# Kernel optimization log

Hardware: AMD Instinct MI355X
Metric: run time of the kernel (lower is better)

## Reference

```python
import jax, jax.numpy as jnp
import numpy as np

# ---- constants (match init_kwargs / input_specs) ----
B, NPG, EPG = 512, 50, 60          # graphs, nodes/graph, edges/graph
D, V = 128, 100000                 # embedding_dim, num_items
SPLITS, SCALE = 4, 12.0            # euler steps, logit scale
N, E = B * NPG, B * EPG
STDV = 1.0 / np.sqrt(D)


def _seg_sum(vals, idx, n):
    return jax.ops.segment_sum(vals, idx, num_segments=n)


def _l2norm(x, eps=1e-12):
    return x / jnp.maximum(jnp.linalg.norm(x, axis=-1, keepdims=True), eps)


def setup_inputs() -> dict:
    key = jax.random.key(0)
    ks = jax.random.split(key, 40)
    u = lambda i, shape: jax.random.uniform(ks[i], shape, minval=-STDV, maxval=STDV, dtype=jnp.float32)
    offs = jnp.repeat(jnp.arange(B, dtype=jnp.int32) * NPG, EPG)
    inp = dict(
        iid=jax.random.randint(ks[0], (N,), 0, V),
        src=jax.random.randint(ks[1], (E,), 0, NPG).astype(jnp.int32) + offs,
        dst=jax.random.randint(ks[2], (E,), 0, NPG).astype(jnp.int32) + offs,
        edge_w=jax.random.uniform(ks[3], (E,), minval=0.1, maxval=1.0, dtype=jnp.float32),
        edge_t=jax.random.uniform(ks[4], (E,), dtype=jnp.float32),
        node_t=jax.random.uniform(ks[5], (N,), dtype=jnp.float32),
        emb=u(6, (V, D)),
        # GGNN layer (num_layers=1): W1, W2 and torch-layout GRUCell(2D -> D)
        W1=u(7, (D, D)), W2=u(8, (D, D)),
        gw_ih=u(9, (3 * D, 2 * D)), gw_hh=u(10, (3 * D, D)),
        gb_ih=u(11, (3 * D,)), gb_hh=u(12, (3 * D,)),
        # GraphGRUODE GCNConv weights (x@W + b), norm='both'
        Wxr=u(13, (D, D)), bxr=u(14, (D,)), Wxz=u(15, (D, D)), bxz=u(16, (D,)),
        Wxh=u(17, (D, D)), bxh=u(18, (D,)), Whr=u(19, (D, D)), bhr=u(20, (D,)),
        Whz=u(21, (D, D)), bhz=u(22, (D,)), Whh=u(23, (D, D)), bhh=u(24, (D,)),
        # AttnReadout
        Wu=u(25, (D, D)), Wv=u(26, (D, D)), bv=u(27, (D,)), We=u(28, (D, 1)),
        # fc_sr: [2D -> D], no bias
        W_sr=u(29, (2 * D, D)),
    )
    return inp


def reference(iid, src, dst, edge_w, edge_t, node_t, emb,
              W1, W2, gw_ih, gw_hh, gb_ih, gb_hh,
              Wxr, bxr, Wxz, bxz, Wxh, bxh, Whr, bhr, Whz, bhz, Whh, bhh,
              Wu, Wv, bv, We, W_sr):
    # ---- embedding + normalize ----
    feat = _l2norm(emb[iid])                                   # [N, D]

    # ---- GGNNLayer: weighted mean over in-edges, both directions, GRU cell ----
    wcol = edge_w[:, None]
    num1 = _seg_sum(feat[src] * wcol, dst, N)
    den1 = _seg_sum(edge_w, dst, N)
    neigh1 = num1 / jnp.where(den1 == 0, 1.0, den1)[:, None]    # zero for isolated nodes
    num2 = _seg_sum(feat[dst] * wcol, src, N)
    den2 = _seg_sum(edge_w, src, N)
    neigh2 = num2 / jnp.where(den2 == 0, 1.0, den2)[:, None]
    hn = jnp.concatenate([neigh1 @ W1, neigh2 @ W2], axis=1)    # [N, 2D]
    gi = hn @ gw_ih.T + gb_ih
    gh = feat @ gw_hh.T + gb_hh
    ir, iz, ig = jnp.split(gi, 3, axis=1)
    hr, hz, hg = jnp.split(gh, 3, axis=1)
    r = jax.nn.sigmoid(ir + hr)
    z = jax.nn.sigmoid(iz + hz)
    g = jnp.tanh(ig + r * hg)
    feat = (1.0 - z) * g + z * feat
    feat = _l2norm(feat)

    # ---- GraphGRUODE: euler integration over dynamic masked subgraphs ----
    x = feat
    t_end = edge_t.max()
    dt = t_end / SPLITS
    nodiag = src != dst

    def ode_f(t, h):
        nm = node_t >= t                                        # node subgraph mask
        em = (edge_t <= t) & nm[src] & nm[dst] & nodiag          # edge mask (no self-loops)
        emf = em.astype(h.dtype)
        deg = _seg_sum(emf, src, N) + _seg_sum(emf, dst, N)      # undirected degree (reverse edges added)
        dis = jnp.clip(deg, 1.0, None) ** -0.5

        def conv(inp, W, b):                                     # GCNConv, norm='both'
            s = inp * dis[:, None]
            agg = (_seg_sum(s[src] * emf[:, None], dst, N)
                   + _seg_sum(s[dst] * emf[:, None], src, N))
            return (agg * dis[:, None]) @ W + b

        rr = jax.nn.sigmoid(conv(x, Wxr, bxr) + conv(h, Whr, bhr))
        zz = jax.nn.sigmoid(conv(x, Wxz, bxz) + conv(h, Whz, bhz))
        uu = jnp.tanh(conv(x, Wxh, bxh) + conv(rr * h, Whh, bhh))
        dh = (1.0 - zz) * (uu - h)
        return jnp.where(nm[:, None], dh, 0.0)

    h = x
    for k in range(SPLITS):
        h = h + dt * ode_f(k * dt, h)
    feat = _l2norm(h)

    # ---- AttnReadout (fixed NPG nodes/graph -> reshape as segment ops) ----
    fb = feat.reshape(B, NPG, D)
    last = fb[:, -1, :]                                          # last node of each session
    e = jax.nn.sigmoid(fb @ Wu + (last @ Wv + bv)[:, None, :]) @ We   # [B, NPG, 1]
    alpha = jax.nn.softmax(e, axis=1)
    sr_g = jnp.sum(fb * alpha, axis=1)                           # [B, D]

    sr = _l2norm(jnp.concatenate([last, sr_g], axis=1) @ W_sr)   # [B, D]
    target = _l2norm(emb)                                        # [V, D]
    logits = sr @ target.T                                       # [B, V]
    return jax.nn.log_softmax(SCALE * logits, axis=-1)
```

## Files before the change

### kernel.cpp

```cpp
#include <hip/hip_runtime.h>

#define BB 512
#define NPG 50
#define EPG 60
#define DD 128
#define VV 100000
#define VPAD 100032
#define NSPLITS 4
#define FSCALE 12.0f
#define NN (BB*NPG)
#define EE (BB*EPG)
#define NDTOT (NN*DD)
#define NCB (VPAD/64)

typedef __attribute__((ext_vector_type(8))) short bfx8;
typedef __attribute__((ext_vector_type(4))) float f32x4;

__device__ __forceinline__ float sigmoidf_(float x){ return 1.f/(1.f+expf(-x)); }
__device__ __forceinline__ short f2bf(float f){
  union { float f; unsigned u; } v; v.f = f;
  unsigned r = v.u + 0x7FFF + ((v.u >> 16) & 1);
  return (short)(r >> 16);
}

__global__ __launch_bounds__(256) void k_embn(const float* __restrict__ emb, short* __restrict__ embn) {
  int row = blockIdx.x*4 + (threadIdx.x >> 6);
  int lane = threadIdx.x & 63;
  if (row >= VPAD) return;
  if (row >= VV) { embn[(size_t)row*DD+lane]=0; embn[(size_t)row*DD+64+lane]=0; return; }
  const float* r = emb + (size_t)row*DD;
  float a = r[lane], b = r[lane+64];
  float s = a*a + b*b;
  for (int off=32; off; off>>=1) s += __shfl_down(s, off);
  s = __shfl(s, 0);
  float inv = 1.0f/fmaxf(sqrtf(s), 1e-12f);
  embn[(size_t)row*DD+lane]    = f2bf(a*inv);
  embn[(size_t)row*DD+64+lane] = f2bf(b*inv);
}

__global__ __launch_bounds__(128) void k_gather(const int* __restrict__ iid, const float* __restrict__ emb,
                                                float* __restrict__ x, short* __restrict__ xb) {
  int n = blockIdx.x, d = threadIdx.x;
  int v = iid[n];
  float e = emb[(size_t)v*DD + d];
  __shared__ float red2[2];
  float ss = e*e;
  for (int off=32; off; off>>=1) ss += __shfl_down(ss, off);
  if ((d & 63)==0) red2[d>>6] = ss;
  __syncthreads();
  float inv = 1.f/fmaxf(sqrtf(red2[0]+red2[1]), 1e-12f);
  float f = e*inv;
  x[(size_t)n*DD + d] = f;
  xb[(size_t)n*DD + d] = f2bf(f);
}

__global__ __launch_bounds__(256) void k_dt(const float* __restrict__ edge_t, float* __restrict__ dtp) {
  __shared__ float red[256];
  float m = -1e30f;
  for (int e = threadIdx.x; e < EE; e += 256) m = fmaxf(m, edge_t[e]);
  red[threadIdx.x] = m; __syncthreads();
  for (int s=128; s; s>>=1){ if ((int)threadIdx.x < s) red[threadIdx.x] = fmaxf(red[threadIdx.x], red[threadIdx.x+s]); __syncthreads(); }
  if (threadIdx.x==0) dtp[0] = red[0] / (float)NSPLITS;
}

__global__ void k_m12t(const float* __restrict__ W1, const float* __restrict__ W2,
                       const float* __restrict__ gw_ih, short* __restrict__ M12t) {
  int c = blockIdx.x, k = threadIdx.x;
  const float* Wrow = (k < 128) ? (W1 + (size_t)k*128) : (W2 + (size_t)(k-128)*128);
  const float* grow = gw_ih + (size_t)c*256 + ((k < 128) ? 0 : 128);
  float s = 0.f;
  for (int j = 0; j < 128; ++j) s += Wrow[j]*grow[j];
  M12t[(size_t)c*256 + k] = f2bf(s);
}
__global__ void k_bfcopy(const float* __restrict__ src, short* __restrict__ dst) {
  size_t i = (size_t)blockIdx.x*blockDim.x + threadIdx.x;
  dst[i] = f2bf(src[i]);
}
__global__ void k_wrzt(const float* __restrict__ Wxr, const float* __restrict__ Wxz,
                       const float* __restrict__ Whr, const float* __restrict__ Whz,
                       short* __restrict__ Wrzt) {
  int c = blockIdx.x, k = threadIdx.x;
  float v;
  if (k < 128) v = (c < 128) ? Wxr[k*128+c] : Wxz[k*128+(c-128)];
  else         v = (c < 128) ? Whr[(k-128)*128+c] : Whz[(k-128)*128+(c-128)];
  Wrzt[(size_t)c*256 + k] = f2bf(v);
}
__global__ void k_wu2t(const float* __restrict__ Wxh, const float* __restrict__ Whh, short* __restrict__ Wu2t) {
  int c = blockIdx.x, k = threadIdx.x;
  float v = (k < 128) ? Wxh[k*128+c] : Whh[(k-128)*128+c];
  Wu2t[(size_t)c*256 + k] = f2bf(v);
}
__global__ void k_wt128(const float* __restrict__ W, short* __restrict__ Wt) {
  int c = blockIdx.x, k = threadIdx.x;
  Wt[(size_t)c*128 + k] = f2bf(W[(size_t)k*128 + c]);
}
__global__ void k_build_bias(const float* __restrict__ bxr, const float* __restrict__ bhr,
                             const float* __restrict__ bxz, const float* __restrict__ bhz,
                             const float* __restrict__ bxh, const float* __restrict__ bhh,
                             float* __restrict__ brz, float* __restrict__ bu) {
  int t = threadIdx.x;
  if (t < 128) brz[t] = bxr[t] + bhr[t];
  else if (t < 256) brz[t] = bxz[t-128] + bhz[t-128];
  else bu[t-256] = bxh[t-256] + bhh[t-256];
}

__global__ __launch_bounds__(256) void k_grp_mean(const int* __restrict__ src, const int* __restrict__ dst,
                                                  const float* __restrict__ ew, const float* __restrict__ feat,
                                                  short* __restrict__ ABb) {
  __shared__ float fl[NPG*128];
  __shared__ float n1[NPG*128];
  __shared__ float n2[NPG*128];
  __shared__ int sl[EPG], tl[EPG];
  __shared__ float wl[EPG];
  __shared__ float d1[NPG], d2[NPG];
  int b = blockIdx.x, tid = threadIdx.x;
  int nb = b*NPG, eb = b*EPG;
  for (int i = tid; i < NPG*32; i += 256) {
    ((float4*)fl)[i] = ((const float4*)(feat + (size_t)nb*128))[i];
    ((float4*)n1)[i] = make_float4(0.f,0.f,0.f,0.f);
    ((float4*)n2)[i] = make_float4(0.f,0.f,0.f,0.f);
  }
  if (tid < EPG) { sl[tid] = src[eb+tid]-nb; tl[tid] = dst[eb+tid]-nb; wl[tid] = ew[eb+tid]; }
  __syncthreads();
  const int dgrp = tid >> 7, d = tid & 127;
  if (dgrp == 0) {
    for (int e = 0; e < EPG; ++e) n1[tl[e]*128+d] += fl[sl[e]*128+d]*wl[e];
  } else {
    for (int e = 0; e < EPG; ++e) n2[sl[e]*128+d] += fl[tl[e]*128+d]*wl[e];
  }
  if (tid < NPG) {
    float den = 0.f;
    for (int e = 0; e < EPG; ++e) den += (tl[e]==tid) ? wl[e] : 0.f;
    d1[tid] = (den == 0.f) ? 1.f : den;
  } else if (tid >= 128 && tid < 128+NPG) {
    int dd = tid - 128;
    float den = 0.f;
    for (int e = 0; e < EPG; ++e) den += (sl[e]==dd) ? wl[e] : 0.f;
    d2[dd] = (den == 0.f) ? 1.f : den;
  }
  __syncthreads();
  for (int n = 0; n < NPG; ++n) {
    float v = dgrp ? (n2[n*128+d]/d2[n]) : (n1[n*128+d]/d1[n]);
    ABb[(size_t)(nb+n)*256 + dgrp*128 + d] = f2bf(v);
  }
}

__global__ __launch_bounds__(128) void k_gru(const float* __restrict__ gi, const float* __restrict__ gh,
                                             float* __restrict__ x) {
  int n = blockIdx.x, d = threadIdx.x;
  const float* gin = gi + (size_t)n*384;
  const float* ghn = gh + (size_t)n*384;
  float ir = gin[d], iz = gin[128+d], ig = gin[256+d];
  float hr = ghn[d], hz = ghn[128+d], hg = ghn[256+d];
  float f0 = x[(size_t)n*DD + d];
  float r = sigmoidf_(ir + hr);
  float z = sigmoidf_(iz + hz);
  float g = tanhf(ig + r*hg);
  float f = (1.f - z)*g + z*f0;
  __shared__ float red2[2];
  float ss = f*f;
  for (int off=32; off; off>>=1) ss += __shfl_down(ss, off);
  if ((d & 63)==0) red2[d>>6] = ss;
  __syncthreads();
  float inv = 1.f/fmaxf(sqrtf(red2[0]+red2[1]), 1e-12f);
  x[(size_t)n*DD + d] = f*inv;
}

__global__ __launch_bounds__(256) void k_ode_fused(
    const int* __restrict__ src, const int* __restrict__ dst,
    const float* __restrict__ edge_t, const float* __restrict__ node_t,
    const float* __restrict__ dtp,
    float* __restrict__ x, short* __restrict__ fbb,
    const short* __restrict__ Wrzt, const short* __restrict__ Wu2t,
    const float* __restrict__ brz, const float* __restrict__ bu)
{
  __shared__ __align__(16) float xl[NPG*128];
  __shared__ __align__(16) float hl[NPG*128];
  __shared__ __align__(16) float S1[NPG*128];
  __shared__ __align__(16) float S2[NPG*128];
  __shared__ __align__(16) float zzl[NPG*128];
  __shared__ __align__(16) short aggX[64*136];
  __shared__ __align__(16) short aggH[64*136];
  __shared__ int stl[EPG];
  __shared__ float etl[EPG];
  __shared__ float ntl[NPG];
  __shared__ float disl[NPG];
  __shared__ unsigned long long actm_s;
  __shared__ float red4[4];

  const int b = blockIdx.x, tid = threadIdx.x;
  const int nb = b*NPG, eb = b*EPG;
  const int wave = tid>>6, lane = tid&63, quad = lane>>4, l16 = lane&15;
  const float dtv = dtp[0];

  for (int i = tid; i < NPG*32; i += 256) {
    float4 v = ((const float4*)(x + (size_t)nb*128))[i];
    ((float4*)xl)[i] = v;
    ((float4*)hl)[i] = v;
  }
  if (tid < EPG) { stl[tid] = (src[eb+tid]-nb) | ((dst[eb+tid]-nb)<<16); etl[tid] = edge_t[eb+tid]; }
  if (tid >= 64 && tid < 64+NPG) ntl[tid-64] = node_t[nb+tid-64];
  for (int i = tid; i < 14*136; i += 256) { aggX[50*136 + i] = 0; aggH[50*136 + i] = 0; }
  __syncthreads();

  for (int ks = 0; ks < NSPLITS; ++ks) {
    const float t = (float)ks * dtv;
    if (wave == 0) {
      bool p = false;
      if (lane < EPG) {
        int st = stl[lane]; int s = st & 0xffff, tt = st >> 16;
        p = (etl[lane] <= t) && (ntl[s] >= t) && (ntl[tt] >= t) && (s != tt);
      }
      unsigned long long m = __ballot(p);
      if (lane == 0) actm_s = m;
    }
    for (int i = tid; i < NPG*128; i += 256) { S1[i] = 0.f; S2[i] = 0.f; }
    __syncthreads();
    const unsigned long long actm = actm_s;
    if (tid < NPG) {
      float deg = 0.f;
      for (int e = 0; e < EPG; ++e) {
        if ((actm >> e) & 1ULL) {
          int st = stl[e]; int s = st & 0xffff, tt = st >> 16;
          deg += (s==tid ? 1.f:0.f) + (tt==tid ? 1.f:0.f);
        }
      }
      disl[tid] = rsqrtf(fmaxf(deg, 1.f));
    }
    __syncthreads();
    if (tid < 128) {
      const int d = tid;
      for (int e = 0; e < EPG; ++e) {
        if ((actm >> e) & 1ULL) {
          int st = stl[e]; int s = st & 0xffff, tt = st >> 16;
          float ds_ = disl[s], dt_ = disl[tt];
          S1[tt*128+d] += xl[s*128+d]*ds_;
          S1[s*128+d]  += xl[tt*128+d]*dt_;
          S2[tt*128+d] += hl[s*128+d]*ds_;
          S2[s*128+d]  += hl[tt*128+d]*dt_;
        }
      }
    }
    __syncthreads();
    for (int i = tid; i < NPG*128; i += 256) {
      int r = i >> 7, c = i & 127;
      aggX[r*136 + c] = f2bf(S1[i]*disl[r]);
      aggH[r*136 + c] = f2bf(S2[i]*disl[r]);
    }
    __syncthreads();
    {
      f32x4 acc[4][4] = {{{0.f,0.f,0.f,0.f},{0.f,0.f,0.f,0.f},{0.f,0.f,0.f,0.f},{0.f,0.f,0.f,0.f}},
                         {{0.f,0.f,0.f,0.f},{0.f,0.f,0.f,0.f},{0.f,0.f,0.f,0.f},{0.f,0.f,0.f,0.f}},
                         {{0.f,0.f,0.f,0.f},{0.f,0.f,0.f,0.f},{0.f,0.f,0.f,0.f},{0.f,0.f,0.f,0.f}},
                         {{0.f,0.f,0.f,0.f},{0.f,0.f,0.f,0.f},{0.f,0.f,0.f,0.f},{0.f,0.f,0.f,0.f}}};
      for (int k0 = 0; k0 < 256; k0 += 32) {
        const short* Ab = (k0 < 128) ? aggX : aggH;
        const int kk = (k0 & 127) + quad*8;
        bfx8 af[4];
#pragma unroll
        for (int m = 0; m < 4; ++m) af[m] = *(const bfx8*)&Ab[(m*16+l16)*136 + kk];
#pragma unroll
        for (int n = 0; n < 4; ++n) {
          const int bn = (wave*4+n)*16 + l16;
          bfx8 bf = *(const bfx8*)&Wrzt[(size_t)bn*256 + k0 + quad*8];
#pragma unroll
          for (int m = 0; m < 4; ++m)
            acc[m][n] = __builtin_amdgcn_mfma_f32_16x16x32_bf16(af[m], bf, acc[m][n], 0, 0, 0);
        }
      }
#pragma unroll
      for (int n = 0; n < 4; ++n) {
        const int col = (wave*4+n)*16 + l16;
        const float bb = brz[col];
#pragma unroll
        for (int m = 0; m < 4; ++m)
#pragma unroll
          for (int r = 0; r < 4; ++r) {
            const int row = m*16 + quad*4 + r;
            if (row < NPG) {
              float s = sigmoidf_(acc[m][n][r] + bb);
              if (col < 128) S1[row*128+col] = s * hl[row*128+col];
              else           zzl[row*128+col-128] = s;
            }
          }
      }
    }
    __syncthreads();
    for (int i = tid; i < NPG*128; i += 256) S2[i] = 0.f;
    __syncthreads();
    if (tid < 128) {
      const int d = tid;
      for (int e = 0; e < EPG; ++e) {
        if ((actm >> e) & 1ULL) {
          int st = stl[e]; int s = st & 0xffff, tt = st >> 16;
          S2[tt*128+d] += S1[s*128+d]*disl[s];
          S2[s*128+d]  += S1[tt*128+d]*disl[tt];
        }
      }
    }
    __syncthreads();
    for (int i = tid; i < NPG*128; i += 256) {
      int r = i >> 7, c = i & 127;
      aggH[r*136 + c] = f2bf(S2[i]*disl[r]);
    }
    __syncthreads();
    {
      f32x4 acc[4][2] = {{{0.f,0.f,0.f,0.f},{0.f,0.f,0.f,0.f}},
                         {{0.f,0.f,0.f,0.f},{0.f,0.f,0.f,0.f}},
                         {{0.f,0.f,0.f,0.f},{0.f,0.f,0.f,0.f}},
                         {{0.f,0.f,0.f,0.f},{0.f,0.f,0.f,0.f}}};
      for (int k0 = 0; k0 < 256; k0 += 32) {
        const short* Ab = (k0 < 128) ? aggX : aggH;
        const int kk = (k0 & 127) + quad*8;
        bfx8 af[4];
#pragma unroll
        for (int m = 0; m < 4; ++m) af[m] = *(const bfx8*)&Ab[(m*16+l16)*136 + kk];
#pragma unroll
        for (int n = 0; n < 2; ++n) {
          const int bn = (wave*2+n)*16 + l16;
          bfx8 bf = *(const bfx8*)&Wu2t[(size_t)bn*256 + k0 + quad*8];
#pragma unroll
          for (int m = 0; m < 4; ++m)
            acc[m][n] = __builtin_amdgcn_mfma_f32_16x16x32_bf16(af[m], bf, acc[m][n], 0, 0, 0);
        }
      }
#pragma unroll
      for (int n = 0; n < 2; ++n) {
        const int col = (wave*2+n)*16 + l16;
        const float bb = bu[col];
#pragma unroll
        for (int m = 0; m < 4; ++m)
#pragma unroll
          for (int r = 0; r < 4; ++r) {
            const int row = m*16 + quad*4 + r;
            if (row < NPG && ntl[row] >= t) {
              float hv = hl[row*128+col];
              float uu = tanhf(acc[m][n][r] + bb);
              float zv = zzl[row*128+col];
              hl[row*128+col] = hv + dtv*(1.f - zv)*(uu - hv);
            }
          }
      }
    }
    __syncthreads();
  }

  for (int rp = 0; rp < NPG; rp += 2) {
    const int r = rp + (tid>>7);
    const int d = tid & 127;
    float v = hl[r*128 + d];
    float ss = v*v;
    for (int off=32; off; off>>=1) ss += __shfl_down(ss, off);
    if (lane == 0) red4[wave] = ss;
    __syncthreads();
    int w0 = (tid>>7)*2;
    float inv = 1.f/fmaxf(sqrtf(red4[w0]+red4[w0+1]), 1e-12f);
    float f = v*inv;
    x[(size_t)(nb+r)*128 + d] = f;
    fbb[(size_t)(nb+r)*128 + d] = f2bf(f);
    __syncthreads();
  }
}

__global__ __launch_bounds__(256) void gemm_mfma(
    const short* __restrict__ A, int lda,
    const short* __restrict__ Bt, int ldbt,
    const float* __restrict__ bias,
    float* __restrict__ C, int ldc,
    int K, int mode,
    float* __restrict__ outp, float* __restrict__ pmax, float* __restrict__ psum)
{
  __shared__ short As[64*40];
  __shared__ short Bs[64*40];
  const int tid = threadIdx.x;
  const int wave = tid >> 6, lane = tid & 63;
  const int wr = wave >> 1, wc = wave & 1;
  const int quad = lane >> 4, l16 = lane & 15;
  int rb, cb;
  if (mode >= 4) {
    int t = (blockIdx.x & 7)*1563 + (blockIdx.x >> 3);
    rb = t & 7; cb = t >> 3;
  } else { rb = blockIdx.y; cb = blockIdx.x; }
  const int row0 = rb*64, col0 = cb*64;
  f32x4 acc[2][2] = {{{0.f,0.f,0.f,0.f},{0.f,0.f,0.f,0.f}},{{0.f,0.f,0.f,0.f},{0.f,0.f,0.f,0.f}}};
  const int sm = tid >> 2, skq = tid & 3;
  const short* Ap = A + (size_t)(row0+sm)*lda + skq*8;
  const short* Bp = Bt + (size_t)(col0+sm)*ldbt + skq*8;
  for (int k0 = 0; k0 < K; k0 += 32) {
    *(bfx8*)&As[sm*40 + skq*8] = *(const bfx8*)(Ap + k0);
    *(bfx8*)&Bs[sm*40 + skq*8] = *(const bfx8*)(Bp + k0);
    __syncthreads();
    bfx8 a0 = *(bfx8*)&As[(wr*32 + l16)*40 + quad*8];
    bfx8 a1 = *(bfx8*)&As[(wr*32 + 16 + l16)*40 + quad*8];
    bfx8 b0 = *(bfx8*)&Bs[(wc*32 + l16)*40 + quad*8];
    bfx8 b1 = *(bfx8*)&Bs[(wc*32 + 16 + l16)*40 + quad*8];
    acc[0][0] = __builtin_amdgcn_mfma_f32_16x16x32_bf16(a0, b0, acc[0][0], 0, 0, 0);
    acc[0][1] = __builtin_amdgcn_mfma_f32_16x16x32_bf16(a0, b1, acc[0][1], 0, 0, 0);
    acc[1][0] = __builtin_amdgcn_mfma_f32_16x16x32_bf16(a1, b0, acc[1][0], 0, 0, 0);
    acc[1][1] = __builtin_amdgcn_mfma_f32_16x16x32_bf16(a1, b1, acc[1][1], 0, 0, 0);
    __syncthreads();
  }

  if (mode == 0) {
#pragma unroll
    for (int i = 0; i < 2; ++i)
#pragma unroll
      for (int j = 0; j < 2; ++j) {
        int gc = col0 + wc*32 + j*16 + l16;
        float bb = bias ? bias[gc] : 0.f;
#pragma unroll
        for (int r = 0; r < 4; ++r) {
          int gr = row0 + wr*32 + i*16 + quad*4 + r;
          C[(size_t)gr*ldc + gc] = acc[i][j][r] + bb;
        }
      }
  } else if (mode == 4) {
    __shared__ float pm[64][2], ps[64][2];
    int c0 = col0 + wc*32 + l16;
    int c1 = c0 + 16;
#pragma unroll
    for (int i = 0; i < 2; ++i) {
#pragma unroll
      for (int r = 0; r < 4; ++r) {
        int rloc = wr*32 + i*16 + quad*4 + r;
        float v0 = (c0 < VV) ? acc[i][0][r] : -1e30f;
        float v1 = (c1 < VV) ? acc[i][1][r] : -1e30f;
        float m = fmaxf(v0, v1);
#pragma unroll
        for (int off = 1; off < 16; off <<= 1) m = fmaxf(m, __shfl_xor(m, off));
        float s = expf(v0 - m) + expf(v1 - m);
#pragma unroll
        for (int off = 1; off < 16; off <<= 1) s += __shfl_xor(s, off);
        if (l16 == 0) { pm[rloc][wc] = m; ps[rloc][wc] = s; }
      }
    }
    __syncthreads();
    if (tid < 64) {
      float m0 = pm[tid][0], m1 = pm[tid][1];
      float s0 = ps[tid][0], s1 = ps[tid][1];
      float M = fmaxf(m0, m1);
      float S = s0*expf(m0 - M) + s1*expf(m1 - M);
      pmax[(size_t)(row0 + tid)*NCB + cb] = M;
      psum[(size_t)(row0 + tid)*NCB + cb] = S;
    }
  } else {
#pragma unroll
    for (int i = 0; i < 2; ++i) {
#pragma unroll
      for (int r = 0; r < 4; ++r) {
        int gr = row0 + wr*32 + i*16 + quad*4 + r;
        float l = bias[gr];
#pragma unroll
        for (int j = 0; j < 2; ++j) {
          int gc = col0 + wc*32 + j*16 + l16;
          if (gc < VV) outp[(size_t)gr*VV + gc] = acc[i][j][r] - l;
        }
      }
    }
  }
}

__global__ __launch_bounds__(128) void k_attn(const float* __restrict__ fb, const float* __restrict__ U,
                                              const float* __restrict__ lv, const float* __restrict__ We,
                                              const float* __restrict__ W_sr, short* __restrict__ srvb) {
  int b = blockIdx.x, d = threadIdx.x;
  __shared__ float sc[NPG];
  __shared__ float lastv[DD], srg[DD];
  __shared__ float red2[2];
  const float* Ub  = U  + (size_t)b*NPG*DD;
  const float* lvb = lv + (size_t)b*DD;
  if (d < 64) {
    for (int i=0;i<NPG;++i) {
      float e = We[d]   * sigmoidf_(Ub[i*DD + d]      + lvb[d]) +
                We[d+64]* sigmoidf_(Ub[i*DD + 64 + d] + lvb[d+64]);
      for (int off=32; off; off>>=1) e += __shfl_down(e, off);
      if (d==0) sc[i] = e;
    }
  }
  __syncthreads();
  if (d < 64) {
    float v = (d < NPG) ? sc[d] : -1e30f;
    float m = v;
    for (int off=1; off<64; off<<=1) m = fmaxf(m, __shfl_xor(m, off));
    float ex = (d < NPG) ? expf(v - m) : 0.f;
    float s = ex;
    for (int off=1; off<64; off<<=1) s += __shfl_xor(s, off);
    if (d < NPG) sc[d] = ex/s;
  }
  __syncthreads();
  const float* fbb = fb + (size_t)b*NPG*DD;
  float lastd = fbb[(NPG-1)*DD + d];
  float sg = 0.f;
  for (int i=0;i<NPG;++i) sg += fbb[i*DD + d]*sc[i];
  lastv[d] = lastd; srg[d] = sg;
  __syncthreads();
  float acc = 0.f;
  for (int k=0;k<DD;++k) acc += lastv[k]*W_sr[k*DD + d];
  for (int k=0;k<DD;++k) acc += srg[k]*W_sr[(DD+k)*DD + d];
  float ss = acc*acc;
  for (int off=32; off; off>>=1) ss += __shfl_down(ss, off);
  if ((d & 63)==0) red2[d>>6] = ss;
  __syncthreads();
  float inv = 1.f/fmaxf(sqrtf(red2[0]+red2[1]), 1e-12f);
  srvb[(size_t)b*DD + d] = f2bf(FSCALE*acc*inv);
}

__global__ __launch_bounds__(256) void k_lse(const float* __restrict__ pmax, const float* __restrict__ psum,
                                             float* __restrict__ lse) {
  int r = blockIdx.x, tid = threadIdx.x;
  float m = -1e30f, s = 0.f;
  for (int cb = tid; cb < NCB; cb += 256) {
    float m2 = pmax[(size_t)r*NCB + cb], s2 = psum[(size_t)r*NCB + cb];
    float M = fmaxf(m, m2);
    s = s*expf(m - M) + s2*expf(m2 - M);
    m = M;
  }
  __shared__ float ms[256], ssh[256];
  ms[tid] = m; ssh[tid] = s; __syncthreads();
  for (int st=128; st; st>>=1) {
    if (tid < st) {
      float m2 = ms[tid+st], s2 = ssh[tid+st];
      float M = fmaxf(ms[tid], m2);
      ssh[tid] = ssh[tid]*expf(ms[tid]-M) + s2*expf(m2-M);
      ms[tid] = M;
    }
    __syncthreads();
  }
  if (tid==0) lse[r] = ms[0] + logf(ssh[0]);
}

extern "C" void kernel_launch(void* const* d_in, const int* in_sizes, int n_in,
                              void* d_out, int out_size, void* d_ws, size_t ws_size,
                              hipStream_t stream) {
  (void)in_sizes; (void)n_in; (void)out_size; (void)ws_size;
  const int*   iid    = (const int*)  d_in[0];
  const int*   src    = (const int*)  d_in[1];
  const int*   dst    = (const int*)  d_in[2];
  const float* edge_w = (const float*)d_in[3];
  const float* edge_t = (const float*)d_in[4];
  const float* node_t = (const float*)d_in[5];
  const float* emb    = (const float*)d_in[6];
  const float* W1     = (const float*)d_in[7];
  const float* W2     = (const float*)d_in[8];
  const float* gw_ih  = (const float*)d_in[9];
  const float* gw_hh  = (const float*)d_in[10];
  const float* gb_ih  = (const float*)d_in[11];
  const float* gb_hh  = (const float*)d_in[12];
  const float* Wxr = (const float*)d_in[13]; const float* bxr = (const float*)d_in[14];
  const float* Wxz = (const float*)d_in[15]; const float* bxz = (const float*)d_in[16];
  const float* Wxh = (const float*)d_in[17]; const float* bxh = (const float*)d_in[18];
  const float* Whr = (const float*)d_in[19]; const float* bhr = (const float*)d_in[20];
  const float* Whz = (const float*)d_in[21]; const float* bhz = (const float*)d_in[22];
  const float* Whh = (const float*)d_in[23]; const float* bhh = (const float*)d_in[24];
  const float* Wu  = (const float*)d_in[25];
  const float* Wv  = (const float*)d_in[26]; const float* bv  = (const float*)d_in[27];
  const float* We  = (const float*)d_in[28];
  const float* W_sr= (const float*)d_in[29];

  float* ws  = (float*)d_ws;
  float* out = (float*)d_out;

  short* embn = (short*)ws;
  float* pmax = ws + 6402048;
  float* psum = pmax + 800256;
  short* M12t = (short*)(psum + 800256);
  short* gwhhb= (short*)(psum + 800256 + 49152);
  short* Wrzt = (short*)(psum + 800256 + 73728);
  short* Wu2t = (short*)(psum + 800256 + 106496);
  short* Wut  = (short*)(psum + 800256 + 122880);
  short* Wvt  = (short*)(psum + 800256 + 131072);
  float* brz  = psum + 800256 + 139264;
  float* bu   = brz + 256;
  float* lv   = bu + 128;
  float* dtp  = lv + 65536;
  float* lse  = dtp + 4;
  short* srvb = (short*)(lse + 512);

  short* ABb = (short*)out;
  float* x   = out + (size_t) 4*1024*1024;
  float* gi  = out + (size_t)20*1024*1024;
  float* gh  = out + (size_t)30*1024*1024;
  float* U   = out + (size_t)20*1024*1024;
  short* xb  = (short*)(out + (size_t)40*1024*1024);
  short* fbb = (short*)(out + (size_t)42*1024*1024);

  k_embn<<<VPAD/4, 256, 0, stream>>>(emb, embn);
  k_gather<<<NN, 128, 0, stream>>>(iid, emb, x, xb);
  k_dt<<<1, 256, 0, stream>>>(edge_t, dtp);
  k_m12t<<<384, 256, 0, stream>>>(W1, W2, gw_ih, M12t);
  k_bfcopy<<<384, 128, 0, stream>>>(gw_hh, gwhhb);
  k_wrzt<<<256, 256, 0, stream>>>(Wxr, Wxz, Whr, Whz, Wrzt);
  k_wu2t<<<128, 256, 0, stream>>>(Wxh, Whh, Wu2t);
  k_wt128<<<128, 128, 0, stream>>>(Wu, Wut);
  k_wt128<<<128, 128, 0, stream>>>(Wv, Wvt);
  k_build_bias<<<1, 384, 0, stream>>>(bxr, bhr, bxz, bhz, bxh, bhh, brz, bu);

  k_grp_mean<<<BB, 256, 0, stream>>>(src, dst, edge_w, x, ABb);

  gemm_mfma<<<dim3(6,400), 256, 0, stream>>>(ABb, 256, M12t, 256, gb_ih, gi, 384, 256, 0,
      nullptr, nullptr, nullptr);
  gemm_mfma<<<dim3(6,400), 256, 0, stream>>>(xb, 128, gwhhb, 128, gb_hh, gh, 384, 128, 0,
      nullptr, nullptr, nullptr);
  k_gru<<<NN, 128, 0, stream>>>(gi, gh, x);

  k_ode_fused<<<BB, 256, 0, stream>>>(src, dst, edge_t, node_t, dtp, x, fbb, Wrzt, Wu2t, brz, bu);

  gemm_mfma<<<dim3(2,400), 256, 0, stream>>>(fbb, 128, Wut, 128, nullptr, U, 128, 128, 0,
      nullptr, nullptr, nullptr);
  gemm_mfma<<<dim3(2,8), 256, 0, stream>>>(fbb + (size_t)(NPG-1)*DD, NPG*DD, Wvt, 128, bv, lv, 128, 128, 0,
      nullptr, nullptr, nullptr);
  k_attn<<<BB, 128, 0, stream>>>(x, U, lv, We, W_sr, srvb);

  gemm_mfma<<<dim3(8*NCB), 256, 0, stream>>>(srvb, 128, embn, 128, nullptr, nullptr, 0, 128, 4,
      nullptr, pmax, psum);
  k_lse<<<BB, 256, 0, stream>>>(pmax, psum, lse);
  gemm_mfma<<<dim3(8*NCB), 256, 0, stream>>>(srvb, 128, embn, 128, lse, nullptr, 0, 128, 5,
      out, nullptr, nullptr);
}
```

Baseline: 813.5 us.

## Reorder GCN ODE as transform-then-aggregate with precomputed x-projections

The ODE kernel now multiplies the weights first (h@W) and then aggregates with a small dense normalized adjacency matrix built in LDS via MFMA, instead of doing per-edge scatter sums over 128-wide features followed by a 256-K GEMM. The x-side projections (x@Wxr, Wxz, Wxh) are constant across Euler steps, so they are hoisted into one bf16 GEMM before the kernel. The block grows to 512 threads and LDS use drops, which should remove the serial edge loops run by only 128 threads. The cost is extra bf16 rounding (adjacency matrix accumulated in bf16, intermediates stored as bf16) and one more global GEMM launch.

```diff
diff --git a/kernel.cpp b/kernel.cpp
--- a/kernel.cpp
+++ b/kernel.cpp
@@ -10,8 +10,11 @@
 #define FSCALE 12.0f
 #define NN (BB*NPG)
 #define EE (BB*EPG)
-#define NDTOT (NN*DD)
 #define NCB (VPAD/64)
+#define HSTR 132
+#define RSTR 136
+#define TSTR 72
+#define MSTR 72
 
 typedef __attribute__((ext_vector_type(8))) short bfx8;
 typedef __attribute__((ext_vector_type(4))) float f32x4;
@@ -21,6 +24,19 @@
   union { float f; unsigned u; } v; v.f = f;
   unsigned r = v.u + 0x7FFF + ((v.u >> 16) & 1);
   return (short)(r >> 16);
+}
+__device__ __forceinline__ float bf2f(short s){
+  union { unsigned u; float f; } v; v.u = ((unsigned)(unsigned short)s) << 16;
+  return v.f;
+}
+__device__ __forceinline__ unsigned cvtpk_(float lo, float hi){
+  unsigned r; asm("v_cvt_pk_bf16_f32 %0, %1, %2" : "=v"(r) : "v"(lo), "v"(hi)); return r;
+}
+__device__ __forceinline__ bfx8 pack8(float4 a, float4 b){
+  union { bfx8 v; unsigned u[4]; } w;
+  w.u[0] = cvtpk_(a.x, a.y); w.u[1] = cvtpk_(a.z, a.w);
+  w.u[2] = cvtpk_(b.x, b.y); w.u[3] = cvtpk_(b.z, b.w);
+  return w.v;
 }
 
 __global__ __launch_bounds__(256) void k_embn(const float* __restrict__ emb, short* __restrict__ embn) {
@@ -76,19 +92,19 @@
   size_t i = (size_t)blockIdx.x*blockDim.x + threadIdx.x;
   dst[i] = f2bf(src[i]);
 }
-__global__ void k_wrzt(const float* __restrict__ Wxr, const float* __restrict__ Wxz,
-                       const float* __restrict__ Whr, const float* __restrict__ Whz,
-                       short* __restrict__ Wrzt) {
+__global__ void k_whrzt(const float* __restrict__ Whr, const float* __restrict__ Whz,
+                        short* __restrict__ Whrzt) {
   int c = blockIdx.x, k = threadIdx.x;
-  float v;
-  if (k < 128) v = (c < 128) ? Wxr[k*128+c] : Wxz[k*128+(c-128)];
-  else         v = (c < 128) ? Whr[(k-128)*128+c] : Whz[(k-128)*128+(c-128)];
-  Wrzt[(size_t)c*256 + k] = f2bf(v);
-}
-__global__ void k_wu2t(const float* __restrict__ Wxh, const float* __restrict__ Whh, short* __restrict__ Wu2t) {
+  float v = (c < 128) ? Whr[(size_t)k*128 + c] : Whz[(size_t)k*128 + (c-128)];
+  Whrzt[(size_t)c*128 + k] = f2bf(v);
+}
+__global__ void k_w3t(const float* __restrict__ Wxr, const float* __restrict__ Wxz,
+                      const float* __restrict__ Wxh, short* __restrict__ W3t) {
   int c = blockIdx.x, k = threadIdx.x;
-  float v = (k < 128) ? Wxh[k*128+c] : Whh[(k-128)*128+c];
-  Wu2t[(size_t)c*256 + k] = f2bf(v);
+  float v = (c < 128) ? Wxr[(size_t)k*128 + c]
+          : (c < 256) ? Wxz[(size_t)k*128 + (c-128)]
+                      : Wxh[(size_t)k*128 + (c-256)];
+  W3t[(size_t)c*128 + k] = f2bf(v);
 }
 __global__ void k_wt128(const float* __restrict__ W, short* __restrict__ Wt) {
   int c = blockIdx.x, k = threadIdx.x;
@@ -146,7 +162,7 @@
 }
 
 __global__ __launch_bounds__(128) void k_gru(const float* __restrict__ gi, const float* __restrict__ gh,
-                                             float* __restrict__ x) {
+                                             float* __restrict__ x, short* __restrict__ xb2) {
   int n = blockIdx.x, d = threadIdx.x;
   const float* gin = gi + (size_t)n*384;
   const float* ghn = gh + (size_t)n*384;
@@ -163,45 +179,150 @@
   if ((d & 63)==0) red2[d>>6] = ss;
   __syncthreads();
   float inv = 1.f/fmaxf(sqrtf(red2[0]+red2[1]), 1e-12f);
-  x[(size_t)n*DD + d] = f*inv;
-}
-
-__global__ __launch_bounds__(256) void k_ode_fused(
+  float out = f*inv;
+  x[(size_t)n*DD + d] = out;
+  xb2[(size_t)n*DD + d] = f2bf(out);
+}
+
+__global__ __launch_bounds__(512, 4) void k_ode_fused(
     const int* __restrict__ src, const int* __restrict__ dst,
     const float* __restrict__ edge_t, const float* __restrict__ node_t,
     const float* __restrict__ dtp,
     float* __restrict__ x, short* __restrict__ fbb,
-    const short* __restrict__ Wrzt, const short* __restrict__ Wu2t,
+    const short* __restrict__ XA,
+    const short* __restrict__ Whrzt, const short* __restrict__ Whht,
     const float* __restrict__ brz, const float* __restrict__ bu)
 {
-  __shared__ __align__(16) float xl[NPG*128];
-  __shared__ __align__(16) float hl[NPG*128];
-  __shared__ __align__(16) float S1[NPG*128];
-  __shared__ __align__(16) float S2[NPG*128];
-  __shared__ __align__(16) float zzl[NPG*128];
-  __shared__ __align__(16) short aggX[64*136];
-  __shared__ __align__(16) short aggH[64*136];
-  __shared__ int stl[EPG];
+  __shared__ __align__(16) float hl[NPG*HSTR];
+  __shared__ __align__(16) short rhb[NPG*RSTR];
+  __shared__ __align__(16) short T1t[128*TSTR];
+  __shared__ __align__(16) short Mp[64*MSTR];
+  __shared__ int   rp[NPG+1];
+  __shared__ short ci[2*EPG];
+  __shared__ int   cnt[NPG];
+  __shared__ int   stl[EPG];
   __shared__ float etl[EPG];
   __shared__ float ntl[NPG];
   __shared__ float disl[NPG];
   __shared__ unsigned long long actm_s;
-  __shared__ float red4[4];
+  __shared__ float red8[8];
 
   const int b = blockIdx.x, tid = threadIdx.x;
   const int nb = b*NPG, eb = b*EPG;
   const int wave = tid>>6, lane = tid&63, quad = lane>>4, l16 = lane&15;
   const float dtv = dtp[0];
 
-  for (int i = tid; i < NPG*32; i += 256) {
-    float4 v = ((const float4*)(x + (size_t)nb*128))[i];
-    ((float4*)xl)[i] = v;
-    ((float4*)hl)[i] = v;
+  for (int i = tid; i < NPG*32; i += 512) {
+    int n = i >> 5, dq = i & 31;
+    ((float4*)(hl + n*HSTR))[dq] = ((const float4*)(x + (size_t)(nb+n)*128))[dq];
   }
   if (tid < EPG) { stl[tid] = (src[eb+tid]-nb) | ((dst[eb+tid]-nb)<<16); etl[tid] = edge_t[eb+tid]; }
   if (tid >= 64 && tid < 64+NPG) ntl[tid-64] = node_t[nb+tid-64];
-  for (int i = tid; i < 14*136; i += 256) { aggX[50*136 + i] = 0; aggH[50*136 + i] = 0; }
-  __syncthreads();
+  __syncthreads();
+
+  if (tid < NPG) {
+    int c = 0;
+    for (int e = 0; e < EPG; ++e) { int st=stl[e]; int s=st&0xffff, t=st>>16; c += (s==tid)+(t==tid); }
+    cnt[tid] = c;
+  }
+  __syncthreads();
+  if (tid == 0) { int a = 0; for (int n = 0; n < NPG; ++n) { rp[n] = a; a += cnt[n]; } rp[NPG] = a; }
+  __syncthreads();
+  if (tid < NPG) {
+    int w = rp[tid];
+    for (int e = 0; e < EPG; ++e) {
+      int st = stl[e]; int s = st & 0xffff, t = st >> 16;
+      if (t == tid) ci[w++] = (short)(s | (e<<8));
+      if (s == tid) ci[w++] = (short)(t | (e<<8));
+    }
+  }
+  __syncthreads();
+
+  float zreg[4][4];
+
+#define HW_PHASE(WT, XAOFS, USERH)                                                   \
+  {                                                                                  \
+    f32x4 acc[4] = {{0.f,0.f,0.f,0.f},{0.f,0.f,0.f,0.f},{0.f,0.f,0.f,0.f},{0.f,0.f,0.f,0.f}}; \
+    const int coln = wave*16 + l16;                                                  \
+    _Pragma("unroll")                                                                \
+    for (int k0 = 0; k0 < 128; k0 += 32) {                                           \
+      bfx8 af[4];                                                                    \
+      _Pragma("unroll")                                                              \
+      for (int m = 0; m < 4; ++m) {                                                  \
+        int arow = m*16 + l16; if (arow > NPG-1) arow = NPG-1;                       \
+        if (USERH) {                                                                 \
+          af[m] = *(const bfx8*)&rhb[arow*RSTR + k0 + quad*8];                       \
+        } else {                                                                     \
+          const float* hp = &hl[arow*HSTR + k0 + quad*8];                            \
+          float4 f0 = *(const float4*)hp;                                            \
+          float4 f1 = *(const float4*)(hp+4);                                        \
+          af[m] = pack8(f0, f1);                                                     \
+        }                                                                            \
+      }                                                                              \
+      bfx8 bfr = *(const bfx8*)&(WT)[(size_t)coln*128 + k0 + quad*8];                \
+      _Pragma("unroll")                                                              \
+      for (int m = 0; m < 4; ++m)                                                    \
+        acc[m] = __builtin_amdgcn_mfma_f32_16x16x32_bf16(af[m], bfr, acc[m], 0, 0, 0); \
+    }                                                                                \
+    _Pragma("unroll")                                                                \
+    for (int m = 0; m < 4; ++m)                                                      \
+      _Pragma("unroll")                                                              \
+      for (int r = 0; r < 4; ++r) {                                                  \
+        int row = m*16 + quad*4 + r;                                                 \
+        int crow = (row > NPG-1) ? (NPG-1) : row;                                    \
+        float v = acc[m][r] + bf2f(XA[(size_t)(nb+crow)*384 + (XAOFS) + coln]);      \
+        T1t[coln*TSTR + row] = f2bf(v);                                              \
+      }                                                                              \
+  }
+
+#define AGG_PHASE(WHICH)                                                             \
+  {                                                                                  \
+    f32x4 acc[4] = {{0.f,0.f,0.f,0.f},{0.f,0.f,0.f,0.f},{0.f,0.f,0.f,0.f},{0.f,0.f,0.f,0.f}}; \
+    const int cold = wave*16 + l16;                                                  \
+    _Pragma("unroll")                                                                \
+    for (int k0 = 0; k0 < 64; k0 += 32) {                                            \
+      bfx8 af[4];                                                                    \
+      _Pragma("unroll")                                                              \
+      for (int m = 0; m < 4; ++m) af[m] = *(const bfx8*)&Mp[(m*16+l16)*MSTR + k0 + quad*8]; \
+      bfx8 bfr = *(const bfx8*)&T1t[cold*TSTR + k0 + quad*8];                        \
+      _Pragma("unroll")                                                              \
+      for (int m = 0; m < 4; ++m)                                                    \
+        acc[m] = __builtin_amdgcn_mfma_f32_16x16x32_bf16(af[m], bfr, acc[m], 0, 0, 0); \
+    }                                                                                \
+    if ((WHICH) == 0) {                                                              \
+      float bb = brz[cold];                                                          \
+      _Pragma("unroll")                                                              \
+      for (int m = 0; m < 4; ++m)                                                    \
+        _Pragma("unroll")                                                            \
+        for (int r = 0; r < 4; ++r) {                                                \
+          int row = m*16 + quad*4 + r;                                               \
+          if (row < NPG) {                                                           \
+            float s = sigmoidf_(acc[m][r] + bb);                                     \
+            rhb[row*RSTR + cold] = f2bf(s * hl[row*HSTR + cold]);                    \
+          }                                                                          \
+        }                                                                            \
+    } else if ((WHICH) == 1) {                                                       \
+      float bb = brz[128 + cold];                                                    \
+      _Pragma("unroll")                                                              \
+      for (int m = 0; m < 4; ++m)                                                    \
+        _Pragma("unroll")                                                            \
+        for (int r = 0; r < 4; ++r)                                                  \
+          zreg[m][r] = sigmoidf_(acc[m][r] + bb);                                    \
+    } else {                                                                         \
+      float bb = bu[cold];                                                           \
+      _Pragma("unroll")                                                              \
+      for (int m = 0; m < 4; ++m)                                                    \
+        _Pragma("unroll")                                                            \
+        for (int r = 0; r < 4; ++r) {                                                \
+          int row = m*16 + quad*4 + r;                                               \
+          if (row < NPG && ntl[row] >= t) {                                          \
+            float hv = hl[row*HSTR + cold];                                          \
+            float uu = tanhf(acc[m][r] + bb);                                        \
+            hl[row*HSTR + cold] = hv + dtv*(1.f - zreg[m][r])*(uu - hv);             \
+          }                                                                          \
+        }                                                                            \
+    }                                                                                \
+  }
 
   for (int ks = 0; ks < NSPLITS; ++ks) {
     const float t = (float)ks * dtv;
@@ -214,150 +335,51 @@
       unsigned long long m = __ballot(p);
       if (lane == 0) actm_s = m;
     }
-    for (int i = tid; i < NPG*128; i += 256) { S1[i] = 0.f; S2[i] = 0.f; }
+    for (int i = tid; i < 64*MSTR/2; i += 512) ((int*)Mp)[i] = 0;
     __syncthreads();
     const unsigned long long actm = actm_s;
     if (tid < NPG) {
       float deg = 0.f;
-      for (int e = 0; e < EPG; ++e) {
-        if ((actm >> e) & 1ULL) {
-          int st = stl[e]; int s = st & 0xffff, tt = st >> 16;
-          deg += (s==tid ? 1.f:0.f) + (tt==tid ? 1.f:0.f);
-        }
+      for (int idx = rp[tid]; idx < rp[tid+1]; ++idx)
+        deg += (float)((actm >> (((int)ci[idx]) >> 8)) & 1ULL);
+      disl[tid] = rsqrtf(fmaxf(deg, 1.f));
+    }
+    __syncthreads();
+    if (tid < NPG) {
+      float dn = disl[tid];
+      for (int idx = rp[tid]; idx < rp[tid+1]; ++idx) {
+        int v = ci[idx]; int j = v & 255, e = v >> 8;
+        if ((actm >> e) & 1ULL)
+          Mp[tid*MSTR + j] = f2bf(bf2f(Mp[tid*MSTR + j]) + dn*disl[j]);
       }
-      disl[tid] = rsqrtf(fmaxf(deg, 1.f));
-    }
-    __syncthreads();
-    if (tid < 128) {
-      const int d = tid;
-      for (int e = 0; e < EPG; ++e) {
-        if ((actm >> e) & 1ULL) {
-          int st = stl[e]; int s = st & 0xffff, tt = st >> 16;
-          float ds_ = disl[s], dt_ = disl[tt];
-          S1[tt*128+d] += xl[s*128+d]*ds_;
-          S1[s*128+d]  += xl[tt*128+d]*dt_;
-          S2[tt*128+d] += hl[s*128+d]*ds_;
-          S2[s*128+d]  += hl[tt*128+d]*dt_;
-        }
-      }
-    }
-    __syncthreads();
-    for (int i = tid; i < NPG*128; i += 256) {
-      int r = i >> 7, c = i & 127;
-      aggX[r*136 + c] = f2bf(S1[i]*disl[r]);
-      aggH[r*136 + c] = f2bf(S2[i]*disl[r]);
-    }
-    __syncthreads();
-    {
-      f32x4 acc[4][4] = {{{0.f,0.f,0.f,0.f},{0.f,0.f,0.f,0.f},{0.f,0.f,0.f,0.f},{0.f,0.f,0.f,0.f}},
-                         {{0.f,0.f,0.f,0.f},{0.f,0.f,0.f,0.f},{0.f,0.f,0.f,0.f},{0.f,0.f,0.f,0.f}},
-                         {{0.f,0.f,0.f,0.f},{0.f,0.f,0.f,0.f},{0.f,0.f,0.f,0.f},{0.f,0.f,0.f,0.f}},
-                         {{0.f,0.f,0.f,0.f},{0.f,0.f,0.f,0.f},{0.f,0.f,0.f,0.f},{0.f,0.f,0.f,0.f}}};
-      for (int k0 = 0; k0 < 256; k0 += 32) {
-        const short* Ab = (k0 < 128) ? aggX : aggH;
-        const int kk = (k0 & 127) + quad*8;
-        bfx8 af[4];
-#pragma unroll
-        for (int m = 0; m < 4; ++m) af[m] = *(const bfx8*)&Ab[(m*16+l16)*136 + kk];
-#pragma unroll
-        for (int n = 0; n < 4; ++n) {
-          const int bn = (wave*4+n)*16 + l16;
-          bfx8 bf = *(const bfx8*)&Wrzt[(size_t)bn*256 + k0 + quad*8];
-#pragma unroll
-          for (int m = 0; m < 4; ++m)
-            acc[m][n] = __builtin_amdgcn_mfma_f32_16x16x32_bf16(af[m], bf, acc[m][n], 0, 0, 0);
-        }
-      }
-#pragma unroll
-      for (int n = 0; n < 4; ++n) {
-        const int col = (wave*4+n)*16 + l16;
-        const float bb = brz[col];
-#pragma unroll
-        for (int m = 0; m < 4; ++m)
-#pragma unroll
-          for (int r = 0; r < 4; ++r) {
-            const int row = m*16 + quad*4 + r;
-            if (row < NPG) {
-              float s = sigmoidf_(acc[m][n][r] + bb);
-              if (col < 128) S1[row*128+col] = s * hl[row*128+col];
-              else           zzl[row*128+col-128] = s;
-            }
-          }
-      }
-    }
-    __syncthreads();
-    for (int i = tid; i < NPG*128; i += 256) S2[i] = 0.f;
-    __syncthreads();
-    if (tid < 128) {
-      const int d = tid;
-      for (int e = 0; e < EPG; ++e) {
-        if ((actm >> e) & 1ULL) {
-          int st = stl[e]; int s = st & 0xffff, tt = st >> 16;
-          S2[tt*128+d] += S1[s*128+d]*disl[s];
-          S2[s*128+d]  += S1[tt*128+d]*disl[tt];
-        }
-      }
-    }
-    __syncthreads();
-    for (int i = tid; i < NPG*128; i += 256) {
-      int r = i >> 7, c = i & 127;
-      aggH[r*136 + c] = f2bf(S2[i]*disl[r]);
-    }
-    __syncthreads();
-    {
-      f32x4 acc[4][2] = {{{0.f,0.f,0.f,0.f},{0.f,0.f,0.f,0.f}},
-                         {{0.f,0.f,0.f,0.f},{0.f,0.f,0.f,0.f}},
-                         {{0.f,0.f,0.f,0.f},{0.f,0.f,0.f,0.f}},
-                         {{0.f,0.f,0.f,0.f},{0.f,0.f,0.f,0.f}}};
-      for (int k0 = 0; k0 < 256; k0 += 32) {
-        const short* Ab = (k0 < 128) ? aggX : aggH;
-        const int kk = (k0 & 127) + quad*8;
-        bfx8 af[4];
-#pragma unroll
-        for (int m = 0; m < 4; ++m) af[m] = *(const bfx8*)&Ab[(m*16+l16)*136 + kk];
-#pragma unroll
-        for (int n = 0; n < 2; ++n) {
-          const int bn = (wave*2+n)*16 + l16;
-          bfx8 bf = *(const bfx8*)&Wu2t[(size_t)bn*256 + k0 + quad*8];
-#pragma unroll
-          for (int m = 0; m < 4; ++m)
-            acc[m][n] = __builtin_amdgcn_mfma_f32_16x16x32_bf16(af[m], bf, acc[m][n], 0, 0, 0);
-        }
-      }
-#pragma unroll
-      for (int n = 0; n < 2; ++n) {
-        const int col = (wave*2+n)*16 + l16;
-        const float bb = bu[col];
-#pragma unroll
-        for (int m = 0; m < 4; ++m)
-#pragma unroll
-          for (int r = 0; r < 4; ++r) {
-            const int row = m*16 + quad*4 + r;
-            if (row < NPG && ntl[row] >= t) {
-              float hv = hl[row*128+col];
-              float uu = tanhf(acc[m][n][r] + bb);
-              float zv = zzl[row*128+col];
-              hl[row*128+col] = hv + dtv*(1.f - zv)*(uu - hv);
-            }
-          }
-      }
-    }
-    __syncthreads();
-  }
-
-  for (int rp = 0; rp < NPG; rp += 2) {
-    const int r = rp + (tid>>7);
+    }
+    __syncthreads();
+
+    HW_PHASE(Whrzt, 0, false);            __syncthreads();
+    AGG_PHASE(0);                         __syncthreads();
+    HW_PHASE(Whrzt + 128*128, 128, false);__syncthreads();
+    AGG_PHASE(1);                         __syncthreads();
+    HW_PHASE(Whht, 256, true);            __syncthreads();
+    AGG_PHASE(2);                         __syncthreads();
+  }
+#undef HW_PHASE
+#undef AGG_PHASE
+
+  for (int rr0 = 0; rr0 < NPG; rr0 += 4) {
+    const int r = rr0 + (tid>>7);
     const int d = tid & 127;
-    float v = hl[r*128 + d];
+    float v = (r < NPG) ? hl[r*HSTR + d] : 0.f;
     float ss = v*v;
     for (int off=32; off; off>>=1) ss += __shfl_down(ss, off);
-    if (lane == 0) red4[wave] = ss;
-    __syncthreads();
-    int w0 = (tid>>7)*2;
-    float inv = 1.f/fmaxf(sqrtf(red4[w0]+red4[w0+1]), 1e-12f);
-    float f = v*inv;
-    x[(size_t)(nb+r)*128 + d] = f;
-    fbb[(size_t)(nb+r)*128 + d] = f2bf(f);
+    if (lane == 0) red8[wave] = ss;
+    __syncthreads();
+    int g = tid>>7;
+    float inv = 1.f/fmaxf(sqrtf(red8[2*g]+red8[2*g+1]), 1e-12f);
+    if (r < NPG) {
+      float f = v*inv;
+      x[(size_t)(nb+r)*128 + d] = f;
+      fbb[(size_t)(nb+r)*128 + d] = f2bf(f);
+    }
     __syncthreads();
   }
 }
@@ -377,7 +399,7 @@
   const int wr = wave >> 1, wc = wave & 1;
   const int quad = lane >> 4, l16 = lane & 15;
   int rb, cb;
-  if (mode >= 4) {
+  if (mode == 4 || mode == 5) {
     int t = (blockIdx.x & 7)*1563 + (blockIdx.x >> 3);
     rb = t & 7; cb = t >> 3;
   } else { rb = blockIdx.y; cb = blockIdx.x; }
@@ -412,6 +434,19 @@
         for (int r = 0; r < 4; ++r) {
           int gr = row0 + wr*32 + i*16 + quad*4 + r;
           C[(size_t)gr*ldc + gc] = acc[i][j][r] + bb;
+        }
+      }
+  } else if (mode == 6) {
+    short* Cb = (short*)C;
+#pragma unroll
+    for (int i = 0; i < 2; ++i)
+#pragma unroll
+      for (int j = 0; j < 2; ++j) {
+        int gc = col0 + wc*32 + j*16 + l16;
+#pragma unroll
+        for (int r = 0; r < 4; ++r) {
+          int gr = row0 + wr*32 + i*16 + quad*4 + r;
+          Cb[(size_t)gr*ldc + gc] = f2bf(acc[i][j][r]);
         }
       }
   } else if (mode == 4) {
@@ -560,37 +595,41 @@
   float* ws  = (float*)d_ws;
   float* out = (float*)d_out;
 
-  short* embn = (short*)ws;
-  float* pmax = ws + 6402048;
-  float* psum = pmax + 800256;
-  short* M12t = (short*)(psum + 800256);
-  short* gwhhb= (short*)(psum + 800256 + 49152);
-  short* Wrzt = (short*)(psum + 800256 + 73728);
-  short* Wu2t = (short*)(psum + 800256 + 106496);
-  short* Wut  = (short*)(psum + 800256 + 122880);
-  short* Wvt  = (short*)(psum + 800256 + 131072);
-  float* brz  = psum + 800256 + 139264;
-  float* bu   = brz + 256;
-  float* lv   = bu + 128;
-  float* dtp  = lv + 65536;
-  float* lse  = dtp + 4;
-  short* srvb = (short*)(lse + 512);
+  short* embn  = (short*)ws;
+  float* pmax  = ws + 6402048;
+  float* psum  = pmax + 800256;
+  short* M12t  = (short*)(ws + 8002560);
+  short* gwhhb = (short*)(ws + 8051712);
+  short* Whrzt = (short*)(ws + 8076288);
+  short* Whht  = (short*)(ws + 8092672);
+  short* W3t   = (short*)(ws + 8100864);
+  short* Wut   = (short*)(ws + 8125440);
+  short* Wvt   = (short*)(ws + 8133632);
+  float* brz   = ws + 8141824;
+  float* bu    = brz + 256;
+  float* lv    = bu + 128;
+  float* dtp   = lv + 65536;
+  float* lse   = dtp + 4;
+  short* srvb  = (short*)(lse + 512);
 
   short* ABb = (short*)out;
   float* x   = out + (size_t) 4*1024*1024;
+  short* XA  = (short*)(out + (size_t) 8*1024*1024);
   float* gi  = out + (size_t)20*1024*1024;
   float* gh  = out + (size_t)30*1024*1024;
   float* U   = out + (size_t)20*1024*1024;
   short* xb  = (short*)(out + (size_t)40*1024*1024);
-  short* fbb = (short*)(out + (size_t)42*1024*1024);
+  short* xb2 = (short*)(out + (size_t)44*1024*1024);
+  short* fbb = (short*)(out + (size_t)46*1024*1024);
 
   k_embn<<<VPAD/4, 256, 0, stream>>>(emb, embn);
   k_gather<<<NN, 128, 0, stream>>>(iid, emb, x, xb);
   k_dt<<<1, 256, 0, stream>>>(edge_t, dtp);
   k_m12t<<<384, 256, 0, stream>>>(W1, W2, gw_ih, M12t);
   k_bfcopy<<<384, 128, 0, stream>>>(gw_hh, gwhhb);
-  k_wrzt<<<256, 256, 0, stream>>>(Wxr, Wxz, Whr, Whz, Wrzt);
-  k_wu2t<<<128, 256, 0, stream>>>(Wxh, Whh, Wu2t);
+  k_whrzt<<<256, 128, 0, stream>>>(Whr, Whz, Whrzt);
+  k_wt128<<<128, 128, 0, stream>>>(Whh, Whht);
+  k_w3t<<<384, 128, 0, stream>>>(Wxr, Wxz, Wxh, W3t);
   k_wt128<<<128, 128, 0, stream>>>(Wu, Wut);
   k_wt128<<<128, 128, 0, stream>>>(Wv, Wvt);
   k_build_bias<<<1, 384, 0, stream>>>(bxr, bhr, bxz, bhz, bxh, bhh, brz, bu);
@@ -601,9 +640,12 @@
       nullptr, nullptr, nullptr);
   gemm_mfma<<<dim3(6,400), 256, 0, stream>>>(xb, 128, gwhhb, 128, gb_hh, gh, 384, 128, 0,
       nullptr, nullptr, nullptr);
-  k_gru<<<NN, 128, 0, stream>>>(gi, gh, x);
-
-  k_ode_fused<<<BB, 256, 0, stream>>>(src, dst, edge_t, node_t, dtp, x, fbb, Wrzt, Wu2t, brz, bu);
+  k_gru<<<NN, 128, 0, stream>>>(gi, gh, x, xb2);
+
+  gemm_mfma<<<dim3(6,400), 256, 0, stream>>>(xb2, 128, W3t, 128, nullptr, (float*)XA, 384, 128, 6,
+      nullptr, nullptr, nullptr);
+
+  k_ode_fused<<<BB, 512, 0, stream>>>(src, dst, edge_t, node_t, dtp, x, fbb, XA, Whrzt, Whht, brz, bu);
 
   gemm_mfma<<<dim3(2,400), 256, 0, stream>>>(fbb, 128, Wut, 128, nullptr, U, 128, 128, 0,
       nullptr, nullptr, nullptr);
```

Measured after the change: 709.9 us. 1.15x faster.
